# Performance work log

Hardware: AMD Instinct MI355X
Metric: run time of the kernel (lower is better)

The kernel has to match this reference:

```python
import jax, jax.numpy as jnp
import numpy as np


def setup_inputs() -> dict:
    key = jax.random.key(0)
    ks = jax.random.split(key, 5)
    B, T, I, H = 64, 2048, 128, 128
    bound = 1.0 / np.sqrt(H)
    x = jax.random.normal(ks[0], (B, T, I), dtype=jnp.float32)
    W_xh = jax.random.uniform(ks[1], (H, I), minval=-bound, maxval=bound, dtype=jnp.float32)
    b_xh = jax.random.uniform(ks[2], (H,), minval=-bound, maxval=bound, dtype=jnp.float32)
    W_hh = jax.random.uniform(ks[3], (H, H), minval=-bound, maxval=bound, dtype=jnp.float32)
    b_hh = jax.random.uniform(ks[4], (H,), minval=-bound, maxval=bound, dtype=jnp.float32)
    return {"x": x, "W_xh": W_xh, "b_xh": b_xh, "W_hh": W_hh, "b_hh": b_hh}


def reference(x, W_xh, b_xh, W_hh, b_hh):
    # x: [B, T, I]; nn.Linear applies x @ W.T + b.
    # Precompute the input projection for all timesteps in one GEMM.
    xp = jnp.einsum('bti,hi->bth', x, W_xh) + b_xh  # [B, T, H]
    B = x.shape[0]
    H = W_hh.shape[0]
    h0 = jnp.zeros((B, H), dtype=x.dtype)

    def step(h, xt):
        h_new = jnp.tanh(xt + h @ W_hh.T + b_hh)
        return h_new, h_new

    h_last, hs = jax.lax.scan(step, h0, jnp.swapaxes(xp, 0, 1))  # hs: [T, B, H]
    h_seq = jnp.swapaxes(hs, 0, 1)  # [B, T, H]
    return h_seq, h_last[None]  # h: [1, B, H]
```

## Files before the change

kernel.cpp:

```cpp
#include <hip/hip_runtime.h>

#define B_ 64
#define T_ 2048
#define I_ 128
#define H_ 128
#define CHUNK 128
#define NCHUNK (T_ / CHUNK)

typedef _Float16 half2v __attribute__((ext_vector_type(2)));

__device__ __forceinline__ float fdot2(unsigned h, unsigned w, float acc) {
#if __has_builtin(__builtin_amdgcn_fdot2)
    return __builtin_amdgcn_fdot2(__builtin_bit_cast(half2v, h),
                                  __builtin_bit_cast(half2v, w), acc, false);
#else
    half2v a = __builtin_bit_cast(half2v, h);
    half2v b = __builtin_bit_cast(half2v, w);
    acc = fmaf((float)a.x, (float)b.x, acc);
    return fmaf((float)a.y, (float)b.y, acc);
#endif
}

__device__ __forceinline__ unsigned pkh(float a, float b) {
    half2v v; v.x = (_Float16)a; v.y = (_Float16)b;
    return __builtin_bit_cast(unsigned, v);
}

__global__ __launch_bounds__(256) void xp_gemm(
    const float* __restrict__ x, const float* __restrict__ Wxh,
    const float* __restrict__ bxh, float* __restrict__ xp)
{
    __shared__ float ws[H_ * I_];
    const int tid = threadIdx.x;
    {
        const float4* src = (const float4*)Wxh;
        float4* dst = (float4*)ws;
        #pragma unroll
        for (int i = 0; i < (H_ * I_ / 4) / 256; ++i)
            dst[tid + i * 256] = src[tid + i * 256];
    }
    __syncthreads();

    const int r0 = (tid >> 4) * 8;
    const int c0 = (tid & 15) * 8;
    const float* xb = x + ((size_t)blockIdx.x * 128 + r0) * I_;
    const float* wb = ws + c0 * I_;

    float acc[8][8];
    #pragma unroll
    for (int i = 0; i < 8; ++i)
        #pragma unroll
        for (int j = 0; j < 8; ++j) acc[i][j] = 0.f;

    float4 xa[8], wa[8], xn[8], wn[8];
    #pragma unroll
    for (int i = 0; i < 8; ++i) xa[i] = *(const float4*)(xb + i * I_);
    #pragma unroll
    for (int j = 0; j < 8; ++j) wa[j] = *(const float4*)(wb + j * I_);

    for (int k4 = 0; k4 < 32; k4 += 2) {
        #pragma unroll
        for (int i = 0; i < 8; ++i) xn[i] = *(const float4*)(xb + i * I_ + k4 * 4 + 4);
        #pragma unroll
        for (int j = 0; j < 8; ++j) wn[j] = *(const float4*)(wb + j * I_ + k4 * 4 + 4);
        #pragma unroll
        for (int i = 0; i < 8; ++i)
            #pragma unroll
            for (int j = 0; j < 8; ++j) {
                acc[i][j] = fmaf(xa[i].x, wa[j].x, acc[i][j]);
                acc[i][j] = fmaf(xa[i].y, wa[j].y, acc[i][j]);
                acc[i][j] = fmaf(xa[i].z, wa[j].z, acc[i][j]);
                acc[i][j] = fmaf(xa[i].w, wa[j].w, acc[i][j]);
            }
        if (k4 + 2 < 32) {
            #pragma unroll
            for (int i = 0; i < 8; ++i) xa[i] = *(const float4*)(xb + i * I_ + k4 * 4 + 8);
            #pragma unroll
            for (int j = 0; j < 8; ++j) wa[j] = *(const float4*)(wb + j * I_ + k4 * 4 + 8);
        }
        #pragma unroll
        for (int i = 0; i < 8; ++i)
            #pragma unroll
            for (int j = 0; j < 8; ++j) {
                acc[i][j] = fmaf(xn[i].x, wn[j].x, acc[i][j]);
                acc[i][j] = fmaf(xn[i].y, wn[j].y, acc[i][j]);
                acc[i][j] = fmaf(xn[i].z, wn[j].z, acc[i][j]);
                acc[i][j] = fmaf(xn[i].w, wn[j].w, acc[i][j]);
            }
    }

    const float4 b0 = *(const float4*)(bxh + c0);
    const float4 b1 = *(const float4*)(bxh + c0 + 4);
    float* orow = xp + ((size_t)blockIdx.x * 128 + r0) * H_ + c0;
    #pragma unroll
    for (int i = 0; i < 8; ++i) {
        float4 o0, o1;
        o0.x = acc[i][0] + b0.x; o0.y = acc[i][1] + b0.y;
        o0.z = acc[i][2] + b0.z; o0.w = acc[i][3] + b0.w;
        o1.x = acc[i][4] + b1.x; o1.y = acc[i][5] + b1.y;
        o1.z = acc[i][6] + b1.z; o1.w = acc[i][7] + b1.w;
        *(float4*)(orow + i * H_) = o0;
        *(float4*)(orow + i * H_ + 4) = o1;
    }
}

__device__ __forceinline__ void stage_chunk64(const float* __restrict__ g,
                                              float* l, int ln)
{
    #pragma unroll
    for (int i = 0; i < 64; ++i) {
        const int off = i * 256;
        __builtin_amdgcn_global_load_lds(
            (const __attribute__((address_space(1))) unsigned int*)(g + off + ln * 4),
            (__attribute__((address_space(3))) unsigned int*)(l + off),
            16, 0, 0);
    }
}

#define G16(M) M(0) M(1) M(2) M(3) M(4) M(5) M(6) M(7) \
               M(8) M(9) M(10) M(11) M(12) M(13) M(14) M(15)

#define DECLW(g) unsigned wa##g##_0, wa##g##_1, wa##g##_2, wa##g##_3, \
                          wb##g##_0, wb##g##_1, wb##g##_2, wb##g##_3;
#define LOADW(g) { \
    const float4 xA0 = *(const float4*)(rowA + 8 * g);     \
    const float4 xA1 = *(const float4*)(rowA + 8 * g + 4); \
    wa##g##_0 = pkh(xA0.x, xA0.y); wa##g##_1 = pkh(xA0.z, xA0.w); \
    wa##g##_2 = pkh(xA1.x, xA1.y); wa##g##_3 = pkh(xA1.z, xA1.w); \
    const float4 xB0 = *(const float4*)(rowB + 8 * g);     \
    const float4 xB1 = *(const float4*)(rowB + 8 * g + 4); \
    wb##g##_0 = pkh(xB0.x, xB0.y); wb##g##_1 = pkh(xB0.z, xB0.w); \
    wb##g##_2 = pkh(xB1.x, xB1.y); wb##g##_3 = pkh(xB1.z, xB1.w); }

#define DECLH(g) uint4 hv##g;
#define READH(g) hv##g = hbp[g];
#define DOTG(g) \
    a00 = fdot2(hv##g.x, wa##g##_0, a00); a01 = fdot2(hv##g.y, wa##g##_1, a01); \
    a00 = fdot2(hv##g.z, wa##g##_2, a00); a01 = fdot2(hv##g.w, wa##g##_3, a01); \
    a10 = fdot2(hv##g.x, wb##g##_0, a10); a11 = fdot2(hv##g.y, wb##g##_1, a11); \
    a10 = fdot2(hv##g.z, wb##g##_2, a10); a11 = fdot2(hv##g.w, wb##g##_3, a11);

__global__ __launch_bounds__(64, 1) void rnn_scan(
    const float* __restrict__ Whh, const float* __restrict__ bhh,
    float* __restrict__ seq , float* __restrict__ hlast)
{
    __shared__ float xpl[2][CHUNK * H_];
    __shared__ unsigned hpk[2][64];

    const int l = threadIdx.x;
    const int b = blockIdx.x;
    const int j0 = 2 * l;

    const float* rowA = Whh + (size_t)j0 * H_;
    const float* rowB = Whh + (size_t)(j0 + 1) * H_;

    G16(DECLW)
    G16(LOADW)

    const float2 bj = *(const float2*)&bhh[j0];
    const float bj0 = bj.x, bj1 = bj.y;
    hpk[0][l] = 0u;
    hpk[1][l] = 0u;

    float* xp = seq + (size_t)b * T_ * H_;
    stage_chunk64(xp, &xpl[0][0], l);

    float h0 = 0.f, h1 = 0.f;
    int tg = 0;
    for (int c = 0; c < NCHUNK; ++c) {
        asm volatile("s_waitcnt vmcnt(0)" ::: "memory");
        if (c + 1 < NCHUNK)
            stage_chunk64(xp + (size_t)(c + 1) * CHUNK * H_, &xpl[(c + 1) & 1][0], l);

        const float* xb = &xpl[c & 1][0];
        float* sq = xp + (size_t)c * CHUNK * H_;

        for (int t = 0; t < CHUNK; ++t, ++tg) {
            const uint4* hbp = (const uint4*)&hpk[tg & 1][0];
            G16(DECLH)
            G16(READH)
            float a00 = bj0, a01 = 0.f, a10 = bj1, a11 = 0.f;
            G16(DOTG)
            const float2 xc = *(const float2*)&xb[t * H_ + j0];
            const float p0 = xc.x + a00 + a01;
            const float p1 = xc.y + a10 + a11;
            const float e0 = exp2f(p0 * 2.8853900817779268f);
            const float e1 = exp2f(p1 * 2.8853900817779268f);
            h0 = 1.f - 2.f * __builtin_amdgcn_rcpf(e0 + 1.f);
            h1 = 1.f - 2.f * __builtin_amdgcn_rcpf(e1 + 1.f);
            hpk[(tg & 1) ^ 1][l] = pkh(h0, h1);
            *(float2*)&sq[t * H_ + j0] = make_float2(h0, h1);
        }
    }
    *(float2*)&hlast[b * H_ + j0] = make_float2(h0, h1);
}

extern "C" void kernel_launch(void* const* d_in, const int* in_sizes, int n_in,
                              void* d_out, int out_size, void* d_ws, size_t ws_size,
                              hipStream_t stream)
{
    const float* x   = (const float*)d_in[0];
    const float* Wxh = (const float*)d_in[1];
    const float* bxh = (const float*)d_in[2];
    const float* Whh = (const float*)d_in[3];
    const float* bhh = (const float*)d_in[4];
    float* out   = (float*)d_out;
    float* hlast = out + (size_t)B_ * T_ * H_;

    xp_gemm<<<(B_ * T_) / 128, 256, 0, stream>>>(x, Wxh, bxh, out);
    rnn_scan<<<B_, 64, 0, stream>>>(Whh, bhh, out, hlast);
}
```

Measured before the change: 1.208 ms.

## Split recurrent scan across two waves with one hidden unit per thread

The scan kernel now launches 128 threads per batch row, each computing one hidden unit instead of two. This halves the serial fdot2 chain per timestep. The cost is a workgroup barrier after every step to exchange the fp16 hidden state between the two waves. Chunk staging of the precomputed input projection is split across both waves, and inline asm pins the packed weights in VGPRs.

Result: faster. 966.8 us (-20.0%).

```diff
diff --git a/kernel.cpp b/kernel.cpp
--- a/kernel.cpp
+++ b/kernel.cpp
@@ -104,12 +104,12 @@
     }
 }
 
-__device__ __forceinline__ void stage_chunk64(const float* __restrict__ g,
-                                              float* l, int ln)
-{
-    #pragma unroll
-    for (int i = 0; i < 64; ++i) {
-        const int off = i * 256;
+__device__ __forceinline__ void stage_chunk128(const float* __restrict__ g,
+                                               float* l, int wv, int ln)
+{
+    #pragma unroll
+    for (int i = 0; i < 32; ++i) {
+        const int off = i * 512 + wv * 256;
         __builtin_amdgcn_global_load_lds(
             (const __attribute__((address_space(1))) unsigned int*)(g + off + ln * 4),
             (__attribute__((address_space(3))) unsigned int*)(l + off),
@@ -120,79 +120,71 @@
 #define G16(M) M(0) M(1) M(2) M(3) M(4) M(5) M(6) M(7) \
                M(8) M(9) M(10) M(11) M(12) M(13) M(14) M(15)
 
-#define DECLW(g) unsigned wa##g##_0, wa##g##_1, wa##g##_2, wa##g##_3, \
-                          wb##g##_0, wb##g##_1, wb##g##_2, wb##g##_3;
+#define DECLW(g) unsigned w##g##_0, w##g##_1, w##g##_2, w##g##_3;
 #define LOADW(g) { \
-    const float4 xA0 = *(const float4*)(rowA + 8 * g);     \
-    const float4 xA1 = *(const float4*)(rowA + 8 * g + 4); \
-    wa##g##_0 = pkh(xA0.x, xA0.y); wa##g##_1 = pkh(xA0.z, xA0.w); \
-    wa##g##_2 = pkh(xA1.x, xA1.y); wa##g##_3 = pkh(xA1.z, xA1.w); \
-    const float4 xB0 = *(const float4*)(rowB + 8 * g);     \
-    const float4 xB1 = *(const float4*)(rowB + 8 * g + 4); \
-    wb##g##_0 = pkh(xB0.x, xB0.y); wb##g##_1 = pkh(xB0.z, xB0.w); \
-    wb##g##_2 = pkh(xB1.x, xB1.y); wb##g##_3 = pkh(xB1.z, xB1.w); }
-
-#define DECLH(g) uint4 hv##g;
-#define READH(g) hv##g = hbp[g];
-#define DOTG(g) \
-    a00 = fdot2(hv##g.x, wa##g##_0, a00); a01 = fdot2(hv##g.y, wa##g##_1, a01); \
-    a00 = fdot2(hv##g.z, wa##g##_2, a00); a01 = fdot2(hv##g.w, wa##g##_3, a01); \
-    a10 = fdot2(hv##g.x, wb##g##_0, a10); a11 = fdot2(hv##g.y, wb##g##_1, a11); \
-    a10 = fdot2(hv##g.z, wb##g##_2, a10); a11 = fdot2(hv##g.w, wb##g##_3, a11);
-
-__global__ __launch_bounds__(64, 1) void rnn_scan(
+    const float4 f0 = *(const float4*)(row + 8 * g);     \
+    const float4 f1 = *(const float4*)(row + 8 * g + 4); \
+    w##g##_0 = pkh(f0.x, f0.y); w##g##_1 = pkh(f0.z, f0.w); \
+    w##g##_2 = pkh(f1.x, f1.y); w##g##_3 = pkh(f1.z, f1.w); }
+#define PINW(g) asm("" : "+v"(w##g##_0), "+v"(w##g##_1), "+v"(w##g##_2), "+v"(w##g##_3));
+#define STEPG(g) { \
+    const uint4 hv = hbp[g]; \
+    a0 = fdot2(hv.x, w##g##_0, a0); \
+    a1 = fdot2(hv.y, w##g##_1, a1); \
+    a2 = fdot2(hv.z, w##g##_2, a2); \
+    a3 = fdot2(hv.w, w##g##_3, a3); }
+
+__global__ __launch_bounds__(128, 1) void rnn_scan(
     const float* __restrict__ Whh, const float* __restrict__ bhh,
     float* __restrict__ seq , float* __restrict__ hlast)
 {
     __shared__ float xpl[2][CHUNK * H_];
-    __shared__ unsigned hpk[2][64];
-
-    const int l = threadIdx.x;
-    const int b = blockIdx.x;
-    const int j0 = 2 * l;
-
-    const float* rowA = Whh + (size_t)j0 * H_;
-    const float* rowB = Whh + (size_t)(j0 + 1) * H_;
-
+    __shared__ _Float16 hf[2][H_];
+
+    const int tid = threadIdx.x;
+    const int j   = tid;
+    const int b   = blockIdx.x;
+    const int wv  = tid >> 6;
+    const int ln  = tid & 63;
+
+    const float* row = Whh + (size_t)j * H_;
     G16(DECLW)
     G16(LOADW)
-
-    const float2 bj = *(const float2*)&bhh[j0];
-    const float bj0 = bj.x, bj1 = bj.y;
-    hpk[0][l] = 0u;
-    hpk[1][l] = 0u;
+    G16(PINW)
+
+    const float bj = bhh[j];
+    hf[0][j] = (_Float16)0.f;
+    hf[1][j] = (_Float16)0.f;
 
     float* xp = seq + (size_t)b * T_ * H_;
-    stage_chunk64(xp, &xpl[0][0], l);
-
-    float h0 = 0.f, h1 = 0.f;
+    stage_chunk128(xp, &xpl[0][0], wv, ln);
+
+    float h = 0.f;
     int tg = 0;
     for (int c = 0; c < NCHUNK; ++c) {
-        asm volatile("s_waitcnt vmcnt(0)" ::: "memory");
+        asm volatile("s_waitcnt vmcnt(0) lgkmcnt(0)" ::: "memory");
+        __builtin_amdgcn_s_barrier();
         if (c + 1 < NCHUNK)
-            stage_chunk64(xp + (size_t)(c + 1) * CHUNK * H_, &xpl[(c + 1) & 1][0], l);
+            stage_chunk128(xp + (size_t)(c + 1) * CHUNK * H_, &xpl[(c + 1) & 1][0], wv, ln);
 
         const float* xb = &xpl[c & 1][0];
         float* sq = xp + (size_t)c * CHUNK * H_;
 
         for (int t = 0; t < CHUNK; ++t, ++tg) {
-            const uint4* hbp = (const uint4*)&hpk[tg & 1][0];
-            G16(DECLH)
-            G16(READH)
-            float a00 = bj0, a01 = 0.f, a10 = bj1, a11 = 0.f;
-            G16(DOTG)
-            const float2 xc = *(const float2*)&xb[t * H_ + j0];
-            const float p0 = xc.x + a00 + a01;
-            const float p1 = xc.y + a10 + a11;
-            const float e0 = exp2f(p0 * 2.8853900817779268f);
-            const float e1 = exp2f(p1 * 2.8853900817779268f);
-            h0 = 1.f - 2.f * __builtin_amdgcn_rcpf(e0 + 1.f);
-            h1 = 1.f - 2.f * __builtin_amdgcn_rcpf(e1 + 1.f);
-            hpk[(tg & 1) ^ 1][l] = pkh(h0, h1);
-            *(float2*)&sq[t * H_ + j0] = make_float2(h0, h1);
+            const uint4* hbp = (const uint4*)&hf[tg & 1][0];
+            float a0 = bj, a1 = 0.f, a2 = 0.f, a3 = 0.f;
+            G16(STEPG)
+            const float xc = xb[t * H_ + j];
+            const float p = xc + ((a0 + a1) + (a2 + a3));
+            const float e = exp2f(p * 2.8853900817779268f);
+            h = 1.f - 2.f * __builtin_amdgcn_rcpf(e + 1.f);
+            hf[(tg & 1) ^ 1][j] = (_Float16)h;
+            sq[t * H_ + j] = h;
+            asm volatile("s_waitcnt lgkmcnt(0)" ::: "memory");
+            __builtin_amdgcn_s_barrier();
         }
     }
-    *(float2*)&hlast[b * H_ + j0] = make_float2(h0, h1);
+    hlast[b * H_ + j] = h;
 }
 
 extern "C" void kernel_launch(void* const* d_in, const int* in_sizes, int n_in,
@@ -208,5 +200,5 @@
     float* hlast = out + (size_t)B_ * T_ * H_;
 
     xp_gemm<<<(B_ * T_) / 128, 256, 0, stream>>>(x, Wxh, bxh, out);
-    rnn_scan<<<B_, 64, 0, stream>>>(Whh, bhh, out, hlast);
-}
+    rnn_scan<<<B_, 128, 0, stream>>>(Whh, bhh, out, hlast);
+}
```

## Broadcast hidden state via readlane instead of LDS double buffer

Applied to the files above, without the earlier changes.

Replaces the per-step exchange of the packed fp16 hidden state through a shared-memory double buffer with 64 v_readlane broadcasts from the owning lanes into scalar registers. The weights are re-laid out so each lane holds the pair for column k matching lane k, and they are pinned in VGPRs. The aim is to drop the LDS write/read round trip and its latency from the serial recurrence critical path. The cost is 64 readlane instructions per step, each a VALU-to-SGPR transfer with possible dependency stalls.

Measured after the change: 1.591 ms. +31.7%, slower.

```diff
diff --git a/kernel.cpp b/kernel.cpp
--- a/kernel.cpp
+++ b/kernel.cpp
@@ -117,35 +117,30 @@
     }
 }
 
-#define G16(M) M(0) M(1) M(2) M(3) M(4) M(5) M(6) M(7) \
-               M(8) M(9) M(10) M(11) M(12) M(13) M(14) M(15)
-
-#define DECLW(g) unsigned wa##g##_0, wa##g##_1, wa##g##_2, wa##g##_3, \
-                          wb##g##_0, wb##g##_1, wb##g##_2, wb##g##_3;
-#define LOADW(g) { \
-    const float4 xA0 = *(const float4*)(rowA + 8 * g);     \
-    const float4 xA1 = *(const float4*)(rowA + 8 * g + 4); \
-    wa##g##_0 = pkh(xA0.x, xA0.y); wa##g##_1 = pkh(xA0.z, xA0.w); \
-    wa##g##_2 = pkh(xA1.x, xA1.y); wa##g##_3 = pkh(xA1.z, xA1.w); \
-    const float4 xB0 = *(const float4*)(rowB + 8 * g);     \
-    const float4 xB1 = *(const float4*)(rowB + 8 * g + 4); \
-    wb##g##_0 = pkh(xB0.x, xB0.y); wb##g##_1 = pkh(xB0.z, xB0.w); \
-    wb##g##_2 = pkh(xB1.x, xB1.y); wb##g##_3 = pkh(xB1.z, xB1.w); }
-
-#define DECLH(g) uint4 hv##g;
-#define READH(g) hv##g = hbp[g];
-#define DOTG(g) \
-    a00 = fdot2(hv##g.x, wa##g##_0, a00); a01 = fdot2(hv##g.y, wa##g##_1, a01); \
-    a00 = fdot2(hv##g.z, wa##g##_2, a00); a01 = fdot2(hv##g.w, wa##g##_3, a01); \
-    a10 = fdot2(hv##g.x, wb##g##_0, a10); a11 = fdot2(hv##g.y, wb##g##_1, a11); \
-    a10 = fdot2(hv##g.z, wb##g##_2, a10); a11 = fdot2(hv##g.w, wb##g##_3, a11);
+#define G64(M) M(0) M(1) M(2) M(3) M(4) M(5) M(6) M(7) M(8) M(9) \
+  M(10) M(11) M(12) M(13) M(14) M(15) M(16) M(17) M(18) M(19) \
+  M(20) M(21) M(22) M(23) M(24) M(25) M(26) M(27) M(28) M(29) \
+  M(30) M(31) M(32) M(33) M(34) M(35) M(36) M(37) M(38) M(39) \
+  M(40) M(41) M(42) M(43) M(44) M(45) M(46) M(47) M(48) M(49) \
+  M(50) M(51) M(52) M(53) M(54) M(55) M(56) M(57) M(58) M(59) \
+  M(60) M(61) M(62) M(63)
+
+#define DECLW(k) unsigned wA##k, wB##k;
+#define LOADW(k) { \
+    const float2 fa = *(const float2*)(rowA + 2 * (k)); \
+    const float2 fb = *(const float2*)(rowB + 2 * (k)); \
+    wA##k = pkh(fa.x, fa.y); wB##k = pkh(fb.x, fb.y); }
+#define PINW(k) asm("" : "+v"(wA##k), "+v"(wB##k));
+#define STG(k) { \
+    const unsigned hk = (unsigned)__builtin_amdgcn_readlane((int)hcur, (k)); \
+    if (((k) & 1) == 0) { aA0 = fdot2(hk, wA##k, aA0); aB0 = fdot2(hk, wB##k, aB0); } \
+    else                { aA1 = fdot2(hk, wA##k, aA1); aB1 = fdot2(hk, wB##k, aB1); } }
 
 __global__ __launch_bounds__(64, 1) void rnn_scan(
     const float* __restrict__ Whh, const float* __restrict__ bhh,
     float* __restrict__ seq , float* __restrict__ hlast)
 {
     __shared__ float xpl[2][CHUNK * H_];
-    __shared__ unsigned hpk[2][64];
 
     const int l = threadIdx.x;
     const int b = blockIdx.x;
@@ -154,19 +149,18 @@
     const float* rowA = Whh + (size_t)j0 * H_;
     const float* rowB = Whh + (size_t)(j0 + 1) * H_;
 
-    G16(DECLW)
-    G16(LOADW)
+    G64(DECLW)
+    G64(LOADW)
+    G64(PINW)
 
     const float2 bj = *(const float2*)&bhh[j0];
     const float bj0 = bj.x, bj1 = bj.y;
-    hpk[0][l] = 0u;
-    hpk[1][l] = 0u;
 
     float* xp = seq + (size_t)b * T_ * H_;
     stage_chunk64(xp, &xpl[0][0], l);
 
+    unsigned hcur = 0u;
     float h0 = 0.f, h1 = 0.f;
-    int tg = 0;
     for (int c = 0; c < NCHUNK; ++c) {
         asm volatile("s_waitcnt vmcnt(0)" ::: "memory");
         if (c + 1 < NCHUNK)
@@ -175,20 +169,17 @@
         const float* xb = &xpl[c & 1][0];
         float* sq = xp + (size_t)c * CHUNK * H_;
 
-        for (int t = 0; t < CHUNK; ++t, ++tg) {
-            const uint4* hbp = (const uint4*)&hpk[tg & 1][0];
-            G16(DECLH)
-            G16(READH)
-            float a00 = bj0, a01 = 0.f, a10 = bj1, a11 = 0.f;
-            G16(DOTG)
+        for (int t = 0; t < CHUNK; ++t) {
             const float2 xc = *(const float2*)&xb[t * H_ + j0];
-            const float p0 = xc.x + a00 + a01;
-            const float p1 = xc.y + a10 + a11;
+            float aA0 = bj0, aA1 = 0.f, aB0 = bj1, aB1 = 0.f;
+            G64(STG)
+            const float p0 = xc.x + aA0 + aA1;
+            const float p1 = xc.y + aB0 + aB1;
             const float e0 = exp2f(p0 * 2.8853900817779268f);
             const float e1 = exp2f(p1 * 2.8853900817779268f);
             h0 = 1.f - 2.f * __builtin_amdgcn_rcpf(e0 + 1.f);
             h1 = 1.f - 2.f * __builtin_amdgcn_rcpf(e1 + 1.f);
-            hpk[(tg & 1) ^ 1][l] = pkh(h0, h1);
+            hcur = pkh(h0, h1);
             *(float2*)&sq[t * H_ + j0] = make_float2(h0, h1);
         }
     }
```
